# Optimization experiments

Hardware: AMD Instinct MI355X
Metric: run time of the kernel (lower is better)

The kernel has to match this reference:

```python
import jax, jax.numpy as jnp
import numpy as np

B, S, D = 64, 1024, 1024
NUM_TAGS = 33            # real IOBES tags
N = NUM_TAGS + 1         # + BOS tag
BOS = N - 1
NEG_INF = -10000.0


def setup_inputs() -> dict:
    key = jax.random.key(0)
    k1, k2, k3, k4 = jax.random.split(key, 4)
    emissions = jax.random.normal(k1, (B, S, D), dtype=jnp.float32)
    tags = jax.random.randint(k2, (B, S), 0, NUM_TAGS)          # valid real tags only
    mask = jnp.ones((B, S), dtype=jnp.float32)
    W = jax.random.normal(k3, (D, N), dtype=jnp.float32) / np.sqrt(D)
    b = jnp.zeros((N,), dtype=jnp.float32)
    transitions = jax.random.uniform(k4, (N, N), minval=-0.1, maxval=0.1, dtype=jnp.float32)
    # nothing may transition INTO the BOS tag
    transitions = transitions.at[:, BOS].set(NEG_INF)
    return {"emissions": emissions, "tags": tags, "mask": mask,
            "W": W, "b": b, "transitions": transitions}


def _crf_nll(em, tags, mask, transitions):
    """em: (B,S,N) projected emissions. Returns scalar NLL (sum over batch)."""
    # ---- gold path score ----
    first = tags[:, 0]                                          # (B,)
    score = transitions[BOS, first] + jnp.take_along_axis(em[:, 0], first[:, None], axis=1)[:, 0]
    e_t = jnp.take_along_axis(em[:, 1:], tags[:, 1:, None], axis=2)[..., 0]   # (B,S-1)
    t_t = transitions[tags[:, :-1], tags[:, 1:]]                 # (B,S-1)
    score = score + jnp.sum((e_t + t_t) * mask[:, 1:], axis=1)   # (B,)

    # ---- log partition via forward algorithm (scan over time) ----
    alphas0 = transitions[BOS][None, :] + em[:, 0]               # (B,N)

    def step(alphas, xs):
        em_t, m_t = xs                                           # (B,N), (B,)
        # scores[b, prev, nxt] = alphas[b,prev] + T[prev,nxt] + em_t[b,nxt]
        scores = alphas[:, :, None] + transitions[None] + em_t[:, None, :]
        new = jax.scipy.special.logsumexp(scores, axis=1)        # (B,N)
        m = m_t[:, None]
        return m * new + (1.0 - m) * alphas, None

    xs = (jnp.swapaxes(em[:, 1:], 0, 1), jnp.swapaxes(mask[:, 1:], 0, 1))  # time-major
    alphas, _ = jax.lax.scan(step, alphas0, xs)
    partition = jax.scipy.special.logsumexp(alphas, axis=1)      # (B,)
    return -jnp.sum(score - partition)


def reference(emissions, tags, mask, W, b, transitions):
    proj = emissions @ W + b                                     # (B,S,N), dropout p=0 is identity
    loss = _crf_nll(proj, tags, mask, transitions)
    logits = proj[:, :, :-1]                                     # drop BOS column, as in torch forward
    return loss, logits
```

## Files before the change

### kernel.cpp

```cpp
#include <hip/hip_runtime.h>
#include <math.h>

#define SS 1024
#define DD 1024
#define NB 64
#define NT 34
#define NP 48
#define NC 32
#define BOSR 33

typedef __attribute__((ext_vector_type(8))) short bf16x8;
typedef __attribute__((ext_vector_type(4))) float f32x4;

#define WS_BOS   0
#define WS_PMAT  (WS_BOS + NB*SS)
#define WS_CC    (WS_PMAT + NB*NC*NP*NP)
#define WS_Z     (WS_CC + NB*NC)
#define WS_SC    (WS_Z + NB)
#define WS_BF16  (WS_SC + NB)
#define BW_WT    0
#define BW_ETA   (48*1024)

__device__ __forceinline__ float warp_sum64(float x) {
  #pragma unroll
  for (int off = 32; off > 0; off >>= 1) x += __shfl_down(x, off, 64);
  return x;
}
__device__ __forceinline__ float rfl(float x) {
  return __int_as_float(__builtin_amdgcn_readfirstlane(__float_as_int(x)));
}
__device__ __forceinline__ unsigned short f2bf(float f) {
  unsigned int u = __float_as_uint(f);
  unsigned int r = u + 0x7fffu + ((u >> 16) & 1u);
  return (unsigned short)(r >> 16);
}
__device__ __forceinline__ float bf2f(unsigned short h) {
  return __uint_as_float(((unsigned int)h) << 16);
}
__device__ __forceinline__ unsigned int pk_bf16(float a, float b) {
  unsigned int d;
  asm("v_cvt_pk_bf16_f32 %0, %1, %2" : "=v"(d) : "v"(a), "v"(b));
  return d;
}

__global__ __launch_bounds__(256) void prep(const float* __restrict__ W,
                                            const float* __restrict__ T,
                                            unsigned short* __restrict__ bw) {
  int idx = blockIdx.x * 256 + threadIdx.x;
  if (idx < 48 * 1024) {
    int n = idx >> 10, k = idx & 1023;
    float v = (n < NT) ? W[k * NT + n] : 0.0f;
    bw[BW_WT + idx] = f2bf(v);
  } else if (idx < 48 * 1024 + 48 * 64) {
    int j = idx - 48 * 1024;
    int m = j >> 6, k = j & 63;
    float v = (m < NT && k < NT) ? __expf(T[k * NT + m]) : 0.0f;
    bw[BW_ETA + j] = f2bf(v);
  }
}

__global__ __launch_bounds__(256) void gemm_mfma(
    const float* __restrict__ em, const unsigned short* __restrict__ bw,
    const float* __restrict__ bias,
    float* __restrict__ logits, float* __restrict__ bos) {
  __shared__ unsigned short At[2][128][40];
  const int tid = threadIdx.x;
  const int lane = tid & 63, wv = tid >> 6;
  const int q = lane >> 4, l15 = lane & 15;
  const size_t row0 = (size_t)blockIdx.x * 128;
  const unsigned short* Wt = bw + BW_WT;
  const f32x4* g4 = (const f32x4*)(em + row0 * DD);

  f32x4 acc[2][3];
  f32x4 z4 = {0.f, 0.f, 0.f, 0.f};
  #pragma unroll
  for (int mt = 0; mt < 2; ++mt)
    #pragma unroll
    for (int nt = 0; nt < 3; ++nt) acc[mt][nt] = z4;

  int sr[4], sq[4];
  #pragma unroll
  for (int i = 0; i < 4; ++i) { int s = tid + i * 256; sr[i] = s >> 3; sq[i] = s & 7; }

  f32x4 pf[4];
  #pragma unroll
  for (int i = 0; i < 4; ++i)
    pf[i] = __builtin_nontemporal_load(g4 + sr[i] * 256 + sq[i]);
  bf16x8 Bf[3], Bn[3];
  #pragma unroll
  for (int nt = 0; nt < 3; ++nt)
    Bf[nt] = *(const bf16x8*)(Wt + (nt * 16 + l15) * 1024 + q * 8);

  for (int c = 0; c < 32; ++c) {
    #pragma unroll
    for (int i = 0; i < 4; ++i) {
      uint2 pk;
      pk.x = pk_bf16(pf[i][0], pf[i][1]);
      pk.y = pk_bf16(pf[i][2], pf[i][3]);
      *(uint2*)&At[c & 1][sr[i]][sq[i] * 4] = pk;
    }
    int cn = (c + 1 < 32) ? c + 1 : c;
    #pragma unroll
    for (int i = 0; i < 4; ++i)
      pf[i] = __builtin_nontemporal_load(g4 + sr[i] * 256 + cn * 8 + sq[i]);
    #pragma unroll
    for (int nt = 0; nt < 3; ++nt)
      Bn[nt] = *(const bf16x8*)(Wt + (nt * 16 + l15) * 1024 + cn * 32 + q * 8);
    __syncthreads();
    bf16x8 Af[2];
    #pragma unroll
    for (int mt = 0; mt < 2; ++mt)
      Af[mt] = *(const bf16x8*)&At[c & 1][wv * 32 + mt * 16 + l15][q * 8];
    #pragma unroll
    for (int mt = 0; mt < 2; ++mt)
      #pragma unroll
      for (int nt = 0; nt < 3; ++nt)
        acc[mt][nt] = __builtin_amdgcn_mfma_f32_16x16x32_bf16(
            Af[mt], Bf[nt], acc[mt][nt], 0, 0, 0);
    #pragma unroll
    for (int nt = 0; nt < 3; ++nt) Bf[nt] = Bn[nt];
  }

  #pragma unroll
  for (int nt = 0; nt < 3; ++nt) {
    int col = nt * 16 + l15;
    float bj = (col < NT) ? bias[col] : 0.0f;
    #pragma unroll
    for (int mt = 0; mt < 2; ++mt) {
      #pragma unroll
      for (int r = 0; r < 4; ++r) {
        float v = acc[mt][nt][r] + bj;
        size_t rg = row0 + wv * 32 + mt * 16 + q * 4 + r;
        if (col < 33) logits[rg * 33 + col] = v;
        else if (col == 33) bos[rg] = v;
      }
    }
  }
}

__global__ __launch_bounds__(64) void chains_mat(
    const float* __restrict__ logits, const float* __restrict__ bos,
    const unsigned short* __restrict__ bw, const float* __restrict__ mask,
    const float* __restrict__ T, const int* __restrict__ tags,
    float* __restrict__ Pmat, float* __restrict__ CC,
    float* __restrict__ scorearr) {
  const int blk = blockIdx.x, lane = threadIdx.x;
  if (blk >= NB * NC) {
    int b = blk - NB * NC;
    float local = 0.0f;
    for (int t = lane; t < SS; t += 64) {
      if (t == 0) {
        int tg = tags[b * SS];
        local += T[BOSR * NT + tg] + logits[(size_t)(b * SS) * 33 + tg];
      } else {
        int tg = tags[b * SS + t];
        int tp = tags[b * SS + t - 1];
        float m = mask[b * SS + t];
        local += m * (logits[(size_t)(b * SS + t) * 33 + tg] + T[tp * NT + tg]);
      }
    }
    float w = warp_sum64(local);
    if (lane == 0) scorearr[b] = w;
    return;
  }

  __shared__ unsigned short S[48][72];
  __shared__ float eeL[32][52];
  const int b = blk >> 5, c = blk & 31;
  const int q = lane >> 4, l15 = lane & 15;

  {
    unsigned long long* p = (unsigned long long*)&S[0][0];
    for (int i = lane; i < 864; i += 64) p[i] = 0ull;
  }
  __syncthreads();
  if (lane < NT) S[lane][lane] = 0x3F80;

  int t = c * 32 + 1 + lane;
  float mval = 0.0f;
  if (lane < 32) {
    if (t < SS) {
      size_t rg = (size_t)b * SS + t;
      #pragma unroll
      for (int j = 0; j < 33; ++j) eeL[lane][j] = __expf(logits[rg * 33 + j]);
      eeL[lane][33] = __expf(bos[rg]);
      #pragma unroll
      for (int j = 34; j < 48; ++j) eeL[lane][j] = 0.0f;
      mval = mask[rg];
    } else {
      #pragma unroll
      for (int j = 0; j < 48; ++j) eeL[lane][j] = 0.0f;
    }
  }
  unsigned long long mb = __ballot(mval > 0.5f);

  bf16x8 Af[3][2];
  const unsigned short* eta = bw + BW_ETA;
  #pragma unroll
  for (int mt = 0; mt < 3; ++mt)
    #pragma unroll
    for (int kt = 0; kt < 2; ++kt)
      Af[mt][kt] = *(const bf16x8*)(eta + (mt * 16 + l15) * 64 + kt * 32 + q * 8);

  float Clog = 0.0f;
  __syncthreads();

  for (int tt = 0; tt < 32; ++tt) {
    if ((mb >> tt) & 1ull) {
      bf16x8 Bf[2][3];
      #pragma unroll
      for (int kt = 0; kt < 2; ++kt)
        #pragma unroll
        for (int nt = 0; nt < 3; ++nt)
          Bf[kt][nt] = *(const bf16x8*)&S[nt * 16 + l15][kt * 32 + q * 8];
      f32x4 acc[3][3];
      f32x4 z4 = {0.f, 0.f, 0.f, 0.f};
      #pragma unroll
      for (int mt = 0; mt < 3; ++mt)
        #pragma unroll
        for (int nt = 0; nt < 3; ++nt) {
          acc[mt][nt] = __builtin_amdgcn_mfma_f32_16x16x32_bf16(
              Af[mt][0], Bf[0][nt], z4, 0, 0, 0);
          acc[mt][nt] = __builtin_amdgcn_mfma_f32_16x16x32_bf16(
              Af[mt][1], Bf[1][nt], acc[mt][nt], 0, 0, 0);
        }
      float r = rfl(acc[0][0][0]);
      float rin = __builtin_amdgcn_rcpf(r);
      float Cadd = __logf(r);
      #pragma unroll
      for (int mt = 0; mt < 3; ++mt) {
        f32x4 e4 = *(const f32x4*)&eeL[tt][mt * 16 + q * 4];
        e4 = e4 * rin;
        #pragma unroll
        for (int nt = 0; nt < 3; ++nt) {
          f32x4 v = acc[mt][nt] * e4;
          uint2 pk;
          pk.x = pk_bf16(v[0], v[1]);
          pk.y = pk_bf16(v[2], v[3]);
          *(uint2*)&S[nt * 16 + l15][mt * 16 + q * 4] = pk;
        }
      }
      Clog += Cadd;
      __syncthreads();
    }
  }

  __syncthreads();
  float* Pb = Pmat + (size_t)(b * NC + c) * (NP * NP);
  #pragma unroll
  for (int i = 0; i < 9; ++i) {
    int flat = i * 64 + lane;
    int n = flat / 12, qq = flat - n * 12;
    unsigned long long pk = *(unsigned long long*)&S[n][qq * 4];
    float4 o;
    o.x = bf2f((unsigned short)(pk));
    o.y = bf2f((unsigned short)(pk >> 16));
    o.z = bf2f((unsigned short)(pk >> 32));
    o.w = bf2f((unsigned short)(pk >> 48));
    *(float4*)&Pb[n * 48 + qq * 4] = o;
  }
  if (lane == 0) CC[b * NC + c] = Clog;
}

__global__ __launch_bounds__(64) void reduceZ(
    const float* __restrict__ logits, const float* __restrict__ bos,
    const float* __restrict__ T, const float* __restrict__ Pmat,
    const float* __restrict__ CC, float* __restrict__ Zarr) {
  __shared__ float shv[64];
  const int b = blockIdx.x, lane = threadIdx.x;
  float a0;
  if (lane < 33)       a0 = logits[(size_t)b * SS * 33 + lane] + T[BOSR * NT + lane];
  else if (lane == 33) a0 = bos[(size_t)b * SS] + T[BOSR * NT + 33];
  else                 a0 = -INFINITY;
  float K = rfl(a0);
  float v = (lane < 48) ? __expf(a0 - K) : 0.0f;
  float C = K;
  for (int c = 0; c < NC; ++c) {
    shv[lane] = v;
    __syncthreads();
    float u = 0.0f;
    if (lane < 48) {
      const float* Pr = Pmat + (size_t)(b * NC + c) * (NP * NP) + lane * 48;
      float uu0 = 0.f, uu1 = 0.f, uu2 = 0.f, uu3 = 0.f;
      #pragma unroll
      for (int qq = 0; qq < 12; qq += 4) {
        float4 p0 = *(const float4*)(Pr + qq * 4);
        float4 p1 = *(const float4*)(Pr + qq * 4 + 4);
        float4 p2 = *(const float4*)(Pr + qq * 4 + 8);
        float4 p3 = *(const float4*)(Pr + qq * 4 + 12);
        float4 v0 = *(const float4*)&shv[qq * 4];
        float4 v1 = *(const float4*)&shv[qq * 4 + 4];
        float4 v2 = *(const float4*)&shv[qq * 4 + 8];
        float4 v3 = *(const float4*)&shv[qq * 4 + 12];
        uu0 = fmaf(p0.x, v0.x, uu0); uu0 = fmaf(p0.y, v0.y, uu0);
        uu0 = fmaf(p0.z, v0.z, uu0); uu0 = fmaf(p0.w, v0.w, uu0);
        uu1 = fmaf(p1.x, v1.x, uu1); uu1 = fmaf(p1.y, v1.y, uu1);
        uu1 = fmaf(p1.z, v1.z, uu1); uu1 = fmaf(p1.w, v1.w, uu1);
        uu2 = fmaf(p2.x, v2.x, uu2); uu2 = fmaf(p2.y, v2.y, uu2);
        uu2 = fmaf(p2.z, v2.z, uu2); uu2 = fmaf(p2.w, v2.w, uu2);
        uu3 = fmaf(p3.x, v3.x, uu3); uu3 = fmaf(p3.y, v3.y, uu3);
        uu3 = fmaf(p3.w, v3.w, uu3); uu3 = fmaf(p3.z, v3.z, uu3);
      }
      u = (uu0 + uu1) + (uu2 + uu3);
    }
    float r = rfl(u);
    v = u * __builtin_amdgcn_rcpf(r);
    C += __logf(r) + CC[b * NC + c];
    __syncthreads();
  }
  float s = warp_sum64(v);
  if (lane == 0) Zarr[b] = C + __logf(s);
}

__global__ void finalk(const float* __restrict__ Zarr,
                       const float* __restrict__ sc, float* __restrict__ out) {
  float x = Zarr[threadIdx.x] - sc[threadIdx.x];
  float s = warp_sum64(x);
  if (threadIdx.x == 0) out[0] = s;
}

extern "C" void kernel_launch(void* const* d_in, const int* in_sizes, int n_in,
                              void* d_out, int out_size, void* d_ws, size_t ws_size,
                              hipStream_t stream) {
  const float* em   = (const float*)d_in[0];
  const int*   tags = (const int*)d_in[1];
  const float* mask = (const float*)d_in[2];
  const float* W    = (const float*)d_in[3];
  const float* bias = (const float*)d_in[4];
  const float* T    = (const float*)d_in[5];

  float* out = (float*)d_out;
  float* ws  = (float*)d_ws;
  float* bos   = ws + WS_BOS;
  float* Pmat  = ws + WS_PMAT;
  float* CC    = ws + WS_CC;
  float* Zarr  = ws + WS_Z;
  float* score = ws + WS_SC;
  unsigned short* bw = (unsigned short*)(ws + WS_BF16);
  float* logits = out + 1;

  hipLaunchKernelGGL(prep, dim3(204), dim3(256), 0, stream, W, T, bw);
  hipLaunchKernelGGL(gemm_mfma, dim3(NB * SS / 128), dim3(256), 0, stream,
                     em, bw, bias, logits, bos);
  hipLaunchKernelGGL(chains_mat, dim3(NB * NC + NB), dim3(64), 0, stream,
                     logits, bos, bw, mask, T, tags, Pmat, CC, score);
  hipLaunchKernelGGL(reduceZ, dim3(NB), dim3(64), 0, stream,
                     logits, bos, T, Pmat, CC, Zarr);
  hipLaunchKernelGGL(finalk, dim3(1), dim3(64), 0, stream, Zarr, score, out);
}
```

Baseline: 417.8 us.

## Fuse chunk transfer-matrix products into GEMM epilogue and prefetch Pmat in reduceZ

The projection GEMM now loads emissions straight from global memory into MFMA A-fragments, with no LDS staging or block barriers. Each wave then exponentiates its own 32 rows of logits in shared memory and builds that chunk's 48x48 transfer-matrix product in place, so the separate chains kernel and its re-read of logits are gone. The chunk boundaries shift by one timestep, and t=0 is excluded through the mask bitmask. The gold-path score moves into a second wave of reduceZ, and reduceZ register-prefetches the next Pmat chunk and broadcasts CC with shuffles instead of using barriers. This trades one launch and a global round trip for longer GEMM blocks and more LDS and registers per block, which may lower occupancy.

```diff
diff --git a/kernel.cpp b/kernel.cpp
--- a/kernel.cpp
+++ b/kernel.cpp
@@ -59,17 +59,22 @@
   }
 }
 
-__global__ __launch_bounds__(256) void gemm_mfma(
+__global__ __launch_bounds__(256) void gemm_chains(
     const float* __restrict__ em, const unsigned short* __restrict__ bw,
-    const float* __restrict__ bias,
-    float* __restrict__ logits, float* __restrict__ bos) {
-  __shared__ unsigned short At[2][128][40];
+    const float* __restrict__ bias, const float* __restrict__ mask,
+    float* __restrict__ logits, float* __restrict__ bos,
+    float* __restrict__ Pmat, float* __restrict__ CC) {
+  __shared__ float eeL[4][32][52];
+  __shared__ unsigned short S[4][48][72];
   const int tid = threadIdx.x;
   const int lane = tid & 63, wv = tid >> 6;
   const int q = lane >> 4, l15 = lane & 15;
   const size_t row0 = (size_t)blockIdx.x * 128;
+  const int b = (int)(row0 >> 10);
+  const int cg = (((int)(row0 & 1023)) >> 5) + wv;
   const unsigned short* Wt = bw + BW_WT;
-  const f32x4* g4 = (const f32x4*)(em + row0 * DD);
+
+  const float* A0 = em + (row0 + (size_t)wv * 32 + l15) * DD + q * 8;
 
   f32x4 acc[2][3];
   f32x4 z4 = {0.f, 0.f, 0.f, 0.f};
@@ -78,45 +83,36 @@
     #pragma unroll
     for (int nt = 0; nt < 3; ++nt) acc[mt][nt] = z4;
 
-  int sr[4], sq[4];
-  #pragma unroll
-  for (int i = 0; i < 4; ++i) { int s = tid + i * 256; sr[i] = s >> 3; sq[i] = s & 7; }
-
-  f32x4 pf[4];
-  #pragma unroll
-  for (int i = 0; i < 4; ++i)
-    pf[i] = __builtin_nontemporal_load(g4 + sr[i] * 256 + sq[i]);
+  f32x4 p0a = __builtin_nontemporal_load((const f32x4*)(A0));
+  f32x4 p0b = __builtin_nontemporal_load((const f32x4*)(A0 + 4));
+  f32x4 p1a = __builtin_nontemporal_load((const f32x4*)(A0 + 16 * DD));
+  f32x4 p1b = __builtin_nontemporal_load((const f32x4*)(A0 + 16 * DD + 4));
   bf16x8 Bf[3], Bn[3];
   #pragma unroll
   for (int nt = 0; nt < 3; ++nt)
     Bf[nt] = *(const bf16x8*)(Wt + (nt * 16 + l15) * 1024 + q * 8);
 
   for (int c = 0; c < 32; ++c) {
-    #pragma unroll
-    for (int i = 0; i < 4; ++i) {
-      uint2 pk;
-      pk.x = pk_bf16(pf[i][0], pf[i][1]);
-      pk.y = pk_bf16(pf[i][2], pf[i][3]);
-      *(uint2*)&At[c & 1][sr[i]][sq[i] * 4] = pk;
-    }
-    int cn = (c + 1 < 32) ? c + 1 : c;
-    #pragma unroll
-    for (int i = 0; i < 4; ++i)
-      pf[i] = __builtin_nontemporal_load(g4 + sr[i] * 256 + cn * 8 + sq[i]);
+    int cn = (c + 1 < 32 ? c + 1 : c) * 32;
+    f32x4 n0a = __builtin_nontemporal_load((const f32x4*)(A0 + cn));
+    f32x4 n0b = __builtin_nontemporal_load((const f32x4*)(A0 + cn + 4));
+    f32x4 n1a = __builtin_nontemporal_load((const f32x4*)(A0 + 16 * DD + cn));
+    f32x4 n1b = __builtin_nontemporal_load((const f32x4*)(A0 + 16 * DD + cn + 4));
     #pragma unroll
     for (int nt = 0; nt < 3; ++nt)
-      Bn[nt] = *(const bf16x8*)(Wt + (nt * 16 + l15) * 1024 + cn * 32 + q * 8);
-    __syncthreads();
-    bf16x8 Af[2];
-    #pragma unroll
-    for (int mt = 0; mt < 2; ++mt)
-      Af[mt] = *(const bf16x8*)&At[c & 1][wv * 32 + mt * 16 + l15][q * 8];
-    #pragma unroll
-    for (int mt = 0; mt < 2; ++mt)
-      #pragma unroll
-      for (int nt = 0; nt < 3; ++nt)
-        acc[mt][nt] = __builtin_amdgcn_mfma_f32_16x16x32_bf16(
-            Af[mt], Bf[nt], acc[mt][nt], 0, 0, 0);
+      Bn[nt] = *(const bf16x8*)(Wt + (nt * 16 + l15) * 1024 + cn + q * 8);
+    union { unsigned int u[4]; bf16x8 v; } c0, c1;
+    c0.u[0] = pk_bf16(p0a[0], p0a[1]); c0.u[1] = pk_bf16(p0a[2], p0a[3]);
+    c0.u[2] = pk_bf16(p0b[0], p0b[1]); c0.u[3] = pk_bf16(p0b[2], p0b[3]);
+    c1.u[0] = pk_bf16(p1a[0], p1a[1]); c1.u[1] = pk_bf16(p1a[2], p1a[3]);
+    c1.u[2] = pk_bf16(p1b[0], p1b[1]); c1.u[3] = pk_bf16(p1b[2], p1b[3]);
+    bf16x8 Af0 = c0.v, Af1 = c1.v;
+    #pragma unroll
+    for (int nt = 0; nt < 3; ++nt) {
+      acc[0][nt] = __builtin_amdgcn_mfma_f32_16x16x32_bf16(Af0, Bf[nt], acc[0][nt], 0, 0, 0);
+      acc[1][nt] = __builtin_amdgcn_mfma_f32_16x16x32_bf16(Af1, Bf[nt], acc[1][nt], 0, 0, 0);
+    }
+    p0a = n0a; p0b = n0b; p1a = n1a; p1b = n1b;
     #pragma unroll
     for (int nt = 0; nt < 3; ++nt) Bf[nt] = Bn[nt];
   }
@@ -133,20 +129,95 @@
         size_t rg = row0 + wv * 32 + mt * 16 + q * 4 + r;
         if (col < 33) logits[rg * 33 + col] = v;
         else if (col == 33) bos[rg] = v;
+        eeL[wv][mt * 16 + q * 4 + r][col] = (col < NT) ? __expf(v) : 0.0f;
       }
     }
   }
-}
-
-__global__ __launch_bounds__(64) void chains_mat(
+
+  float mval = 0.0f;
+  if (lane < 32) mval = mask[row0 + wv * 32 + lane];
+  unsigned long long mb = __ballot(mval > 0.5f);
+  if (cg == 0) mb &= ~1ull;
+
+  {
+    unsigned long long* p = (unsigned long long*)&S[wv][0][0];
+    for (int i = lane; i < 864; i += 64) p[i] = 0ull;
+  }
+  if (lane < NT) S[wv][lane][lane] = 0x3F80;
+
+  bf16x8 Ef[3][2];
+  const unsigned short* eta = bw + BW_ETA;
+  #pragma unroll
+  for (int mt = 0; mt < 3; ++mt)
+    #pragma unroll
+    for (int kt = 0; kt < 2; ++kt)
+      Ef[mt][kt] = *(const bf16x8*)(eta + (mt * 16 + l15) * 64 + kt * 32 + q * 8);
+
+  float Clog = 0.0f;
+  for (int tt = 0; tt < 32; ++tt) {
+    if ((mb >> tt) & 1ull) {
+      bf16x8 Bq[2][3];
+      #pragma unroll
+      for (int kt = 0; kt < 2; ++kt)
+        #pragma unroll
+        for (int nt = 0; nt < 3; ++nt)
+          Bq[kt][nt] = *(const bf16x8*)&S[wv][nt * 16 + l15][kt * 32 + q * 8];
+      f32x4 pacc[3][3];
+      #pragma unroll
+      for (int mt = 0; mt < 3; ++mt)
+        #pragma unroll
+        for (int nt = 0; nt < 3; ++nt) {
+          pacc[mt][nt] = __builtin_amdgcn_mfma_f32_16x16x32_bf16(
+              Ef[mt][0], Bq[0][nt], z4, 0, 0, 0);
+          pacc[mt][nt] = __builtin_amdgcn_mfma_f32_16x16x32_bf16(
+              Ef[mt][1], Bq[1][nt], pacc[mt][nt], 0, 0, 0);
+        }
+      float r = rfl(pacc[0][0][0]);
+      float rin = __builtin_amdgcn_rcpf(r);
+      Clog += __logf(r);
+      #pragma unroll
+      for (int mt = 0; mt < 3; ++mt) {
+        f32x4 e4 = *(const f32x4*)&eeL[wv][tt][mt * 16 + q * 4];
+        e4 = e4 * rin;
+        #pragma unroll
+        for (int nt = 0; nt < 3; ++nt) {
+          f32x4 v = pacc[mt][nt] * e4;
+          uint2 pk;
+          pk.x = pk_bf16(v[0], v[1]);
+          pk.y = pk_bf16(v[2], v[3]);
+          *(uint2*)&S[wv][nt * 16 + l15][mt * 16 + q * 4] = pk;
+        }
+      }
+    }
+  }
+
+  float* Pb = Pmat + (size_t)(b * NC + cg) * (NP * NP);
+  #pragma unroll
+  for (int i = 0; i < 9; ++i) {
+    int flat = i * 64 + lane;
+    int n = flat / 12, qq = flat - n * 12;
+    unsigned long long pk = *(unsigned long long*)&S[wv][n][qq * 4];
+    float4 o;
+    o.x = bf2f((unsigned short)(pk));
+    o.y = bf2f((unsigned short)(pk >> 16));
+    o.z = bf2f((unsigned short)(pk >> 32));
+    o.w = bf2f((unsigned short)(pk >> 48));
+    *(float4*)&Pb[n * 48 + qq * 4] = o;
+  }
+  if (lane == 0) CC[b * NC + cg] = Clog;
+}
+
+__global__ __launch_bounds__(128) void reduceZ(
     const float* __restrict__ logits, const float* __restrict__ bos,
-    const unsigned short* __restrict__ bw, const float* __restrict__ mask,
-    const float* __restrict__ T, const int* __restrict__ tags,
-    float* __restrict__ Pmat, float* __restrict__ CC,
+    const float* __restrict__ T, const float* __restrict__ Pmat,
+    const float* __restrict__ CC, const int* __restrict__ tags,
+    const float* __restrict__ mask, float* __restrict__ Zarr,
     float* __restrict__ scorearr) {
-  const int blk = blockIdx.x, lane = threadIdx.x;
-  if (blk >= NB * NC) {
-    int b = blk - NB * NC;
+  const int b = blockIdx.x;
+  const int tid = threadIdx.x;
+  const int lane = tid & 63;
+
+  if (tid >= 64) {
     float local = 0.0f;
     for (int t = lane; t < SS; t += 64) {
       if (t == 0) {
@@ -164,110 +235,7 @@
     return;
   }
 
-  __shared__ unsigned short S[48][72];
-  __shared__ float eeL[32][52];
-  const int b = blk >> 5, c = blk & 31;
-  const int q = lane >> 4, l15 = lane & 15;
-
-  {
-    unsigned long long* p = (unsigned long long*)&S[0][0];
-    for (int i = lane; i < 864; i += 64) p[i] = 0ull;
-  }
-  __syncthreads();
-  if (lane < NT) S[lane][lane] = 0x3F80;
-
-  int t = c * 32 + 1 + lane;
-  float mval = 0.0f;
-  if (lane < 32) {
-    if (t < SS) {
-      size_t rg = (size_t)b * SS + t;
-      #pragma unroll
-      for (int j = 0; j < 33; ++j) eeL[lane][j] = __expf(logits[rg * 33 + j]);
-      eeL[lane][33] = __expf(bos[rg]);
-      #pragma unroll
-      for (int j = 34; j < 48; ++j) eeL[lane][j] = 0.0f;
-      mval = mask[rg];
-    } else {
-      #pragma unroll
-      for (int j = 0; j < 48; ++j) eeL[lane][j] = 0.0f;
-    }
-  }
-  unsigned long long mb = __ballot(mval > 0.5f);
-
-  bf16x8 Af[3][2];
-  const unsigned short* eta = bw + BW_ETA;
-  #pragma unroll
-  for (int mt = 0; mt < 3; ++mt)
-    #pragma unroll
-    for (int kt = 0; kt < 2; ++kt)
-      Af[mt][kt] = *(const bf16x8*)(eta + (mt * 16 + l15) * 64 + kt * 32 + q * 8);
-
-  float Clog = 0.0f;
-  __syncthreads();
-
-  for (int tt = 0; tt < 32; ++tt) {
-    if ((mb >> tt) & 1ull) {
-      bf16x8 Bf[2][3];
-      #pragma unroll
-      for (int kt = 0; kt < 2; ++kt)
-        #pragma unroll
-        for (int nt = 0; nt < 3; ++nt)
-          Bf[kt][nt] = *(const bf16x8*)&S[nt * 16 + l15][kt * 32 + q * 8];
-      f32x4 acc[3][3];
-      f32x4 z4 = {0.f, 0.f, 0.f, 0.f};
-      #pragma unroll
-      for (int mt = 0; mt < 3; ++mt)
-        #pragma unroll
-        for (int nt = 0; nt < 3; ++nt) {
-          acc[mt][nt] = __builtin_amdgcn_mfma_f32_16x16x32_bf16(
-              Af[mt][0], Bf[0][nt], z4, 0, 0, 0);
-          acc[mt][nt] = __builtin_amdgcn_mfma_f32_16x16x32_bf16(
-              Af[mt][1], Bf[1][nt], acc[mt][nt], 0, 0, 0);
-        }
-      float r = rfl(acc[0][0][0]);
-      float rin = __builtin_amdgcn_rcpf(r);
-      float Cadd = __logf(r);
-      #pragma unroll
-      for (int mt = 0; mt < 3; ++mt) {
-        f32x4 e4 = *(const f32x4*)&eeL[tt][mt * 16 + q * 4];
-        e4 = e4 * rin;
-        #pragma unroll
-        for (int nt = 0; nt < 3; ++nt) {
-          f32x4 v = acc[mt][nt] * e4;
-          uint2 pk;
-          pk.x = pk_bf16(v[0], v[1]);
-          pk.y = pk_bf16(v[2], v[3]);
-          *(uint2*)&S[nt * 16 + l15][mt * 16 + q * 4] = pk;
-        }
-      }
-      Clog += Cadd;
-      __syncthreads();
-    }
-  }
-
-  __syncthreads();
-  float* Pb = Pmat + (size_t)(b * NC + c) * (NP * NP);
-  #pragma unroll
-  for (int i = 0; i < 9; ++i) {
-    int flat = i * 64 + lane;
-    int n = flat / 12, qq = flat - n * 12;
-    unsigned long long pk = *(unsigned long long*)&S[n][qq * 4];
-    float4 o;
-    o.x = bf2f((unsigned short)(pk));
-    o.y = bf2f((unsigned short)(pk >> 16));
-    o.z = bf2f((unsigned short)(pk >> 32));
-    o.w = bf2f((unsigned short)(pk >> 48));
-    *(float4*)&Pb[n * 48 + qq * 4] = o;
-  }
-  if (lane == 0) CC[b * NC + c] = Clog;
-}
-
-__global__ __launch_bounds__(64) void reduceZ(
-    const float* __restrict__ logits, const float* __restrict__ bos,
-    const float* __restrict__ T, const float* __restrict__ Pmat,
-    const float* __restrict__ CC, float* __restrict__ Zarr) {
-  __shared__ float shv[64];
-  const int b = blockIdx.x, lane = threadIdx.x;
+  __shared__ __align__(16) float shv[64];
   float a0;
   if (lane < 33)       a0 = logits[(size_t)b * SS * 33 + lane] + T[BOSR * NT + lane];
   else if (lane == 33) a0 = bos[(size_t)b * SS] + T[BOSR * NT + 33];
@@ -275,38 +243,47 @@
   float K = rfl(a0);
   float v = (lane < 48) ? __expf(a0 - K) : 0.0f;
   float C = K;
+  float CCl = (lane < 32) ? CC[b * NC + lane] : 0.0f;
+  const float* Pbase = Pmat + (size_t)b * NC * (NP * NP) + lane * 48;
+
+  f32x4 Pp[12];
+  if (lane < 48) {
+    #pragma unroll
+    for (int i = 0; i < 12; ++i) Pp[i] = *(const f32x4*)(Pbase + i * 4);
+  }
   for (int c = 0; c < NC; ++c) {
     shv[lane] = v;
-    __syncthreads();
+    f32x4 cur[12];
+    #pragma unroll
+    for (int i = 0; i < 12; ++i) cur[i] = Pp[i];
+    if (c + 1 < NC && lane < 48) {
+      #pragma unroll
+      for (int i = 0; i < 12; ++i)
+        Pp[i] = *(const f32x4*)(Pbase + (size_t)(c + 1) * (NP * NP) + i * 4);
+    }
     float u = 0.0f;
     if (lane < 48) {
-      const float* Pr = Pmat + (size_t)(b * NC + c) * (NP * NP) + lane * 48;
       float uu0 = 0.f, uu1 = 0.f, uu2 = 0.f, uu3 = 0.f;
       #pragma unroll
       for (int qq = 0; qq < 12; qq += 4) {
-        float4 p0 = *(const float4*)(Pr + qq * 4);
-        float4 p1 = *(const float4*)(Pr + qq * 4 + 4);
-        float4 p2 = *(const float4*)(Pr + qq * 4 + 8);
-        float4 p3 = *(const float4*)(Pr + qq * 4 + 12);
-        float4 v0 = *(const float4*)&shv[qq * 4];
-        float4 v1 = *(const float4*)&shv[qq * 4 + 4];
-        float4 v2 = *(const float4*)&shv[qq * 4 + 8];
-        float4 v3 = *(const float4*)&shv[qq * 4 + 12];
-        uu0 = fmaf(p0.x, v0.x, uu0); uu0 = fmaf(p0.y, v0.y, uu0);
-        uu0 = fmaf(p0.z, v0.z, uu0); uu0 = fmaf(p0.w, v0.w, uu0);
-        uu1 = fmaf(p1.x, v1.x, uu1); uu1 = fmaf(p1.y, v1.y, uu1);
-        uu1 = fmaf(p1.z, v1.z, uu1); uu1 = fmaf(p1.w, v1.w, uu1);
-        uu2 = fmaf(p2.x, v2.x, uu2); uu2 = fmaf(p2.y, v2.y, uu2);
-        uu2 = fmaf(p2.z, v2.z, uu2); uu2 = fmaf(p2.w, v2.w, uu2);
-        uu3 = fmaf(p3.x, v3.x, uu3); uu3 = fmaf(p3.y, v3.y, uu3);
-        uu3 = fmaf(p3.w, v3.w, uu3); uu3 = fmaf(p3.z, v3.z, uu3);
+        f32x4 v0 = *(const f32x4*)&shv[qq * 4];
+        f32x4 v1 = *(const f32x4*)&shv[qq * 4 + 4];
+        f32x4 v2 = *(const f32x4*)&shv[qq * 4 + 8];
+        f32x4 v3 = *(const f32x4*)&shv[qq * 4 + 12];
+        uu0 = fmaf(cur[qq][0], v0[0], uu0);   uu0 = fmaf(cur[qq][1], v0[1], uu0);
+        uu0 = fmaf(cur[qq][2], v0[2], uu0);   uu0 = fmaf(cur[qq][3], v0[3], uu0);
+        uu1 = fmaf(cur[qq+1][0], v1[0], uu1); uu1 = fmaf(cur[qq+1][1], v1[1], uu1);
+        uu1 = fmaf(cur[qq+1][2], v1[2], uu1); uu1 = fmaf(cur[qq+1][3], v1[3], uu1);
+        uu2 = fmaf(cur[qq+2][0], v2[0], uu2); uu2 = fmaf(cur[qq+2][1], v2[1], uu2);
+        uu2 = fmaf(cur[qq+2][2], v2[2], uu2); uu2 = fmaf(cur[qq+2][3], v2[3], uu2);
+        uu3 = fmaf(cur[qq+3][0], v3[0], uu3); uu3 = fmaf(cur[qq+3][1], v3[1], uu3);
+        uu3 = fmaf(cur[qq+3][2], v3[2], uu3); uu3 = fmaf(cur[qq+3][3], v3[3], uu3);
       }
       u = (uu0 + uu1) + (uu2 + uu3);
     }
     float r = rfl(u);
     v = u * __builtin_amdgcn_rcpf(r);
-    C += __logf(r) + CC[b * NC + c];
-    __syncthreads();
+    C += __logf(r) + __shfl(CCl, c, 64);
   }
   float s = warp_sum64(v);
   if (lane == 0) Zarr[b] = C + __logf(s);
@@ -340,11 +317,9 @@
   float* logits = out + 1;
 
   hipLaunchKernelGGL(prep, dim3(204), dim3(256), 0, stream, W, T, bw);
-  hipLaunchKernelGGL(gemm_mfma, dim3(NB * SS / 128), dim3(256), 0, stream,
-                     em, bw, bias, logits, bos);
-  hipLaunchKernelGGL(chains_mat, dim3(NB * NC + NB), dim3(64), 0, stream,
-                     logits, bos, bw, mask, T, tags, Pmat, CC, score);
-  hipLaunchKernelGGL(reduceZ, dim3(NB), dim3(64), 0, stream,
-                     logits, bos, T, Pmat, CC, Zarr);
+  hipLaunchKernelGGL(gemm_chains, dim3(NB * SS / 128), dim3(256), 0, stream,
+                     em, bw, bias, mask, logits, bos, Pmat, CC);
+  hipLaunchKernelGGL(reduceZ, dim3(NB), dim3(128), 0, stream,
+                     logits, bos, T, Pmat, CC, tags, mask, Zarr, score);
   hipLaunchKernelGGL(finalk, dim3(1), dim3(64), 0, stream, Zarr, score, out);
 }
```

New measurement: 423.1 us. No clear change (+1.3%).
